# Kernel tuning notes

Hardware: AMD Instinct MI355X
Metric: run time of the kernel (lower is better)

The kernel has to match this reference:

```python
import jax, jax.numpy as jnp
import numpy as np

N_STREAMS = 8
DIM = 1024
N_HEADS = 16
HEAD_DIM = DIM // N_HEADS
STREAM_DIM = DIM // N_STREAMS
EPS = 1e-6


def setup_inputs() -> dict:
    key = jax.random.key(0)
    ks = jax.random.split(key, 20)
    B, S, D = 2, 2048, DIM
    inp = {
        "x": jax.random.normal(ks[0], (B, S, D), jnp.float32),
        "rope_cos": jax.random.uniform(ks[1], (S, HEAD_DIM), jnp.float32),
        "rope_sin": jax.random.uniform(ks[2], (S, HEAD_DIM), jnp.float32),
        # DeltaOperator: learned per-channel decay logits
        "delta_decay": jax.random.normal(ks[3], (D,), jnp.float32) * 0.02,
        # gate_proj: Linear(D, 3*n)
        "gate_w": jax.random.normal(ks[4], (3 * N_STREAMS, D), jnp.float32) * 0.02,
        "gate_b": jnp.zeros((3 * N_STREAMS,), jnp.float32),
        "phi_res": jax.random.normal(ks[5], (N_STREAMS, N_STREAMS), jnp.float32) * 0.02,
        "ln1_w": jnp.ones((D,), jnp.float32),
        "ln2_w": jnp.ones((D,), jnp.float32),
        # MLP (StrategicLinear == Linear at inference)
        "w1": jax.random.normal(ks[6], (4 * D, D), jnp.float32) * 0.02,
        "b1": jnp.zeros((4 * D,), jnp.float32),
        "w2": jax.random.normal(ks[7], (D, 4 * D), jnp.float32) * 0.02,
        "b2": jnp.zeros((D,), jnp.float32),
        # nn.MultiheadAttention params
        "in_proj_w": jax.random.normal(ks[8], (3 * D, D), jnp.float32) * 0.02,
        "in_proj_b": jnp.zeros((3 * D,), jnp.float32),
        "out_w": jax.random.normal(ks[9], (D, D), jnp.float32) * 0.02,
        "out_b": jnp.zeros((D,), jnp.float32),
    }
    return inp


def delta_operator(x, decay_logits):
    # out_t = x_t - s_{t-1};  s_t = beta*s_{t-1} + (1-beta)*x_t  (per-channel EMA delta)
    beta = jax.nn.sigmoid(decay_logits)  # [D]

    def step(s, xt):
        out = xt - s
        s_new = beta * s + (1.0 - beta) * xt
        return s_new, out

    xT = jnp.swapaxes(x, 0, 1)  # [S,B,D]
    s0 = jnp.zeros_like(xT[0])
    _, ysT = jax.lax.scan(step, s0, xT)
    return jnp.swapaxes(ysT, 0, 1)  # [B,S,D]


def rms_norm(x, w):
    var = jnp.mean(x * x, axis=-1, keepdims=True)
    return x * jax.lax.rsqrt(var + EPS) * w


def sinkhorn_knopp(phi, iterations=15):
    K = jnp.exp(phi)
    for _ in range(iterations):
        K = K / jnp.sum(K, axis=1, keepdims=True)
        K = K / jnp.sum(K, axis=0, keepdims=True)
    return K


def causal_mha(x, in_proj_w, in_proj_b, out_w, out_b):
    B, S, D = x.shape
    qkv = x @ in_proj_w.T + in_proj_b  # [B,S,3D]
    q, k, v = jnp.split(qkv, 3, axis=-1)
    def heads(t):
        return t.reshape(B, S, N_HEADS, HEAD_DIM).transpose(0, 2, 1, 3)  # [B,H,S,hd]
    q, k, v = heads(q), heads(k), heads(v)
    scores = jnp.einsum("bhqd,bhkd->bhqk", q, k) / jnp.sqrt(jnp.float32(HEAD_DIM))
    mask = jnp.tril(jnp.ones((S, S), bool))
    scores = jnp.where(mask, scores, jnp.float32(-1e9))
    attn = jax.nn.softmax(scores, axis=-1)
    o = jnp.einsum("bhqk,bhkd->bhqd", attn, v)
    o = o.transpose(0, 2, 1, 3).reshape(B, S, D)
    return o @ out_w.T + out_b


def reference(x, rope_cos, rope_sin, delta_decay, gate_w, gate_b, phi_res,
              ln1_w, ln2_w, w1, b1, w2, b2, in_proj_w, in_proj_b, out_w, out_b):
    B, S, D = x.shape
    n = N_STREAMS
    x_delta = delta_operator(x, delta_decay)
    x_state = jnp.mean(x_delta, axis=1)  # [B,D]
    gates = x_state @ gate_w.T + gate_b  # [B,3n]
    g_res = jax.nn.sigmoid(gates[:, 2 * n:])[:, None, :, None]  # [B,1,n,1]
    H_res = sinkhorn_knopp(phi_res, 15)
    x_streams = x_delta.reshape(B, S, n, STREAM_DIM)
    # (x_perm @ H.T).permute back == einsum over stream axis
    mhc_out = jnp.einsum("bsnd,mn->bsmd", x_streams * g_res, H_res).reshape(B, S, D)
    normed = rms_norm(x_delta, ln1_w)
    attn_out = causal_mha(normed, in_proj_w, in_proj_b, out_w, out_b)
    normed2 = rms_norm(x_delta + attn_out, ln2_w)
    h = jax.nn.gelu(normed2 @ w1.T + b1, approximate=False)
    ffn_out = h @ w2.T + b2
    return x_delta + attn_out + ffn_out + mhc_out
```

## Files before the change

kernel.cpp:

```cpp
#include <hip/hip_runtime.h>
#include <hip/hip_bf16.h>
#include <math.h>

#define BB 2
#define SS 2048
#define DDIM 1024
#define NHEAD 16
#define NSTR 8
#define SDIMC 128
#define NCH 16
#define CLEN 128
#define EPSV 1e-6f

using bf16 = __hip_bfloat16;
typedef __attribute__((ext_vector_type(8))) __bf16 bf8;
typedef __attribute__((ext_vector_type(4))) __bf16 bf4v;
typedef __attribute__((ext_vector_type(4))) float f4;

__device__ __forceinline__ bf16 f2b(float v) { return __float2bfloat16(v); }
__device__ __forceinline__ bf8 ld8(const bf16* p) { return *(const bf8*)p; }
__device__ __forceinline__ f4 MFMA(bf8 a, bf8 b, f4 c) {
  return __builtin_amdgcn_mfma_f32_16x16x32_bf16(a, b, c, 0, 0, 0);
}
__device__ __forceinline__ float sigm(float x) { return 1.0f / (1.0f + expf(-x)); }
__device__ __forceinline__ float fexp2(float x) { return __builtin_amdgcn_exp2f(x); }

__device__ __forceinline__ float gelu_f(float v) {
  float x = v * 0.70710678118654752f;
  float ax = fabsf(x);
  float t = __builtin_amdgcn_rcpf(1.0f + 0.3275911f * ax);
  float p = ((((1.061405429f * t - 1.453152027f) * t + 1.421413741f) * t
              - 0.284496736f) * t + 0.254829592f) * t;
  float e = 1.0f - p * fexp2(-ax * ax * 1.4426950408889634f);
  e = copysignf(e, x);
  return 0.5f * v * (1.0f + e);
}

__device__ __forceinline__ void glds16(bf16* l, const bf16* g) {
  __builtin_amdgcn_global_load_lds(
      (const __attribute__((address_space(1))) unsigned int*)g,
      (__attribute__((address_space(3))) unsigned int*)l, 16, 0, 0);
}

__global__ __launch_bounds__(256) void cvt_all(const float* __restrict__ ipw,
                                               const float* __restrict__ ow,
                                               const float* __restrict__ w1,
                                               const float* __restrict__ w2,
                                               bf16* __restrict__ WIPW,
                                               bf16* __restrict__ WOW,
                                               bf16* __restrict__ W1B,
                                               bf16* __restrict__ W2B) {
  const int S1 = 3 * DDIM * DDIM, S2 = S1 + DDIM * DDIM,
            S3 = S2 + 4 * DDIM * DDIM;
  int i4 = (blockIdx.x * 256 + threadIdx.x) * 4;
  const float* src;
  bf16* dst;
  int off;
  if (i4 < S1)      { src = ipw; dst = WIPW; off = i4; }
  else if (i4 < S2) { src = ow;  dst = WOW;  off = i4 - S1; }
  else if (i4 < S3) { src = w1;  dst = W1B;  off = i4 - S2; }
  else              { src = w2;  dst = W2B;  off = i4 - S3; }
  float4 v = *(const float4*)(src + off);
  bf4v o;
  o[0] = (__bf16)v.x; o[1] = (__bf16)v.y; o[2] = (__bf16)v.z; o[3] = (__bf16)v.w;
  *(bf4v*)(dst + off) = o;
}

__global__ __launch_bounds__(256) void delta_passA(const float* __restrict__ x,
                                                   const float* __restrict__ decay,
                                                   float* __restrict__ SA) {
  int idx = blockIdx.x * 256 + threadIdx.x;
  int d = idx % DDIM;
  int c = (idx / DDIM) % NCH;
  int b = idx / (DDIM * NCH);
  float beta = sigm(decay[d]);
  float omb = 1.0f - beta;
  const float* xp = x + ((size_t)(b * SS + c * CLEN)) * DDIM + d;
  float s = 0.0f;
  for (int j = 0; j < CLEN; j++) {
    float xv = xp[(size_t)j * DDIM];
    s = beta * s + omb * xv;
  }
  SA[idx] = s;
}

__global__ __launch_bounds__(256) void delta_passB(const float* __restrict__ SA,
                                                   const float* __restrict__ decay,
                                                   float* __restrict__ SIN) {
  int idx = blockIdx.x * 256 + threadIdx.x;
  int d = idx % DDIM;
  int b = idx / DDIM;
  float beta = sigm(decay[d]);
  float p = beta;
  for (int i = 0; i < 7; i++) p *= p;
  float s = 0.0f;
  for (int c = 0; c < NCH; c++) {
    SIN[(b * NCH + c) * DDIM + d] = s;
    s = p * s + SA[(b * NCH + c) * DDIM + d];
  }
}

__global__ __launch_bounds__(256) void delta_passC(const float* __restrict__ x,
                                                   const float* __restrict__ decay,
                                                   const float* __restrict__ SIN,
                                                   float* __restrict__ XD,
                                                   float* __restrict__ SA) {
  int idx = blockIdx.x * 256 + threadIdx.x;
  int d = idx % DDIM;
  int c = (idx / DDIM) % NCH;
  int b = idx / (DDIM * NCH);
  float beta = sigm(decay[d]);
  float omb = 1.0f - beta;
  const float* xp = x + ((size_t)(b * SS + c * CLEN)) * DDIM + d;
  float* xdp = XD + ((size_t)(b * SS + c * CLEN)) * DDIM + d;
  float s = SIN[idx];
  float sum = 0.0f;
  for (int j = 0; j < CLEN; j++) {
    float xv = xp[(size_t)j * DDIM];
    float o = xv - s;
    xdp[(size_t)j * DDIM] = o;
    sum += o;
    s = beta * s + omb * xv;
  }
  SA[idx] = sum;
}

__global__ __launch_bounds__(1024) void gates_sinkhorn(const float* __restrict__ SA,
                                                       const float* __restrict__ gw,
                                                       const float* __restrict__ gb,
                                                       const float* __restrict__ phi,
                                                       float* __restrict__ gres,
                                                       float* __restrict__ hres) {
  int tid = threadIdx.x;
  int wave = tid >> 6, lane = tid & 63;
  int b = wave >> 3, j = wave & 7;
  float acc = 0.0f;
  for (int d = lane; d < DDIM; d += 64) {
    float xs = 0.0f;
    for (int c = 0; c < NCH; c++) xs += SA[(b * NCH + c) * DDIM + d];
    xs *= (1.0f / (float)SS);
    acc += xs * gw[(2 * NSTR + j) * DDIM + d];
  }
  for (int off = 32; off > 0; off >>= 1) acc += __shfl_down(acc, off);
  if (lane == 0) gres[b * NSTR + j] = sigm(acc + gb[2 * NSTR + j]);
  __syncthreads();
  if (tid == 0) {
    float Km[8][8];
    for (int i = 0; i < 8; i++)
      for (int jj = 0; jj < 8; jj++) Km[i][jj] = expf(phi[i * 8 + jj]);
    for (int it = 0; it < 15; it++) {
      for (int i = 0; i < 8; i++) {
        float rs = 0.0f;
        for (int jj = 0; jj < 8; jj++) rs += Km[i][jj];
        float inv = 1.0f / rs;
        for (int jj = 0; jj < 8; jj++) Km[i][jj] *= inv;
      }
      for (int jj = 0; jj < 8; jj++) {
        float cs = 0.0f;
        for (int i = 0; i < 8; i++) cs += Km[i][jj];
        float inv = 1.0f / cs;
        for (int i = 0; i < 8; i++) Km[i][jj] *= inv;
      }
    }
    for (int i = 0; i < 8; i++)
      for (int jj = 0; jj < 8; jj++) hres[i * 8 + jj] = Km[i][jj];
  }
}

__global__ __launch_bounds__(256) void rmsnorm_k(const float* __restrict__ in,
                                                 const float* __restrict__ w,
                                                 bf16* __restrict__ out) {
  int row = blockIdx.x;
  const float* r = in + (size_t)row * DDIM;
  int tid = threadIdx.x;
  float ss = 0.0f;
  for (int i = tid; i < DDIM; i += 256) {
    float v = r[i];
    ss += v * v;
  }
  for (int off = 32; off > 0; off >>= 1) ss += __shfl_down(ss, off);
  __shared__ float red[4];
  if ((tid & 63) == 0) red[tid >> 6] = ss;
  __syncthreads();
  float tot = red[0] + red[1] + red[2] + red[3];
  float sc = rsqrtf(tot / (float)DDIM + EPSV);
  bf16* o = out + (size_t)row * DDIM;
  for (int i = tid; i < DDIM; i += 256) o[i] = f2b(r[i] * sc * w[i]);
}

template <int ODT, int EPI>
__global__ __launch_bounds__(256) void gemm_lds(const bf16* __restrict__ A,
                                                const bf16* __restrict__ W,
                                                const float* __restrict__ bias,
                                                const float* __restrict__ res,
                                                void* __restrict__ outp,
                                                int M, int N, int K) {
  __shared__ bf16 As[2][128 * 32];
  __shared__ bf16 Bs[2][128 * 32];
  int tid = threadIdx.x;
  int lane = tid & 63, wv = tid >> 6;
  int ml = lane & 15, quad = lane >> 4;
  int wr = wv >> 1, wc = wv & 1;
  int m0 = blockIdx.x * 128, n0 = blockIdx.y * 128;
  const bf16* ga[2];
  const bf16* gb[2];
  int lofs[2];
#pragma unroll
  for (int it = 0; it < 2; it++) {
    int c = it * 256 + tid;
    int row = c >> 2, kc = (c & 3) * 8;
    ga[it] = A + (size_t)(m0 + row) * K + kc;
    gb[it] = W + (size_t)(n0 + row) * K + kc;
    lofs[it] = c * 8;
  }
#pragma unroll
  for (int it = 0; it < 2; it++) {
    glds16(&As[0][lofs[it]], ga[it]);
    glds16(&Bs[0][lofs[it]], gb[it]);
  }
  f4 acc[4][4] = {};
  int nk = K >> 5;
  int cur = 0;
  __syncthreads();
  for (int t = 0; t < nk; t++) {
    if (t + 1 < nk) {
      int ko = (t + 1) * 32;
#pragma unroll
      for (int it = 0; it < 2; it++) {
        glds16(&As[cur ^ 1][lofs[it]], ga[it] + ko);
        glds16(&Bs[cur ^ 1][lofs[it]], gb[it] + ko);
      }
    }
    bf8 af[4], bfr[4];
#pragma unroll
    for (int mi = 0; mi < 4; mi++)
      af[mi] = ld8(&As[cur][(wr * 64 + mi * 16 + ml) * 32 + quad * 8]);
#pragma unroll
    for (int ni = 0; ni < 4; ni++)
      bfr[ni] = ld8(&Bs[cur][(wc * 64 + ni * 16 + ml) * 32 + quad * 8]);
#pragma unroll
    for (int mi = 0; mi < 4; mi++)
#pragma unroll
      for (int ni = 0; ni < 4; ni++)
        acc[mi][ni] = MFMA(af[mi], bfr[ni], acc[mi][ni]);
    __syncthreads();
    cur ^= 1;
  }
#pragma unroll
  for (int mi = 0; mi < 4; mi++)
#pragma unroll
    for (int ni = 0; ni < 4; ni++)
#pragma unroll
      for (int r = 0; r < 4; r++) {
        int row = m0 + wr * 64 + mi * 16 + quad * 4 + r;
        int col = n0 + wc * 64 + ni * 16 + ml;
        size_t idx = (size_t)row * N + col;
        float v = acc[mi][ni][r] + bias[col];
        if (EPI == 1) v = gelu_f(v);
        if (EPI == 2) v += res[idx];
        if (ODT == 1) ((bf16*)outp)[idx] = f2b(v);
        else ((float*)outp)[idx] = v;
      }
}

__global__ __launch_bounds__(256) void gemm_part2(const bf16* __restrict__ A,
                                                  const bf16* __restrict__ W,
                                                  float* __restrict__ P0,
                                                  float* __restrict__ P1,
                                                  int M, int N, int KS, int LDK) {
  __shared__ bf16 As[2][128 * 32];
  __shared__ bf16 Bs[2][128 * 32];
  int tid = threadIdx.x;
  int lane = tid & 63, wv = tid >> 6;
  int ml = lane & 15, quad = lane >> 4;
  int wr = wv >> 1, wc = wv & 1;
  int m0 = blockIdx.x * 128, n0 = blockIdx.y * 128;
  const bf16* Ab = A + blockIdx.z * KS;
  const bf16* Wb = W + blockIdx.z * KS;
  float* P = blockIdx.z ? P1 : P0;
  const bf16* ga[2];
  const bf16* gb[2];
  int lofs[2];
#pragma unroll
  for (int it = 0; it < 2; it++) {
    int c = it * 256 + tid;
    int row = c >> 2, kc = (c & 3) * 8;
    ga[it] = Ab + (size_t)(m0 + row) * LDK + kc;
    gb[it] = Wb + (size_t)(n0 + row) * LDK + kc;
    lofs[it] = c * 8;
  }
#pragma unroll
  for (int it = 0; it < 2; it++) {
    glds16(&As[0][lofs[it]], ga[it]);
    glds16(&Bs[0][lofs[it]], gb[it]);
  }
  f4 acc[4][4] = {};
  int nk = KS >> 5;
  int cur = 0;
  __syncthreads();
  for (int t = 0; t < nk; t++) {
    if (t + 1 < nk) {
      int ko = (t + 1) * 32;
#pragma unroll
      for (int it = 0; it < 2; it++) {
        glds16(&As[cur ^ 1][lofs[it]], ga[it] + ko);
        glds16(&Bs[cur ^ 1][lofs[it]], gb[it] + ko);
      }
    }
    bf8 af[4], bfr[4];
#pragma unroll
    for (int mi = 0; mi < 4; mi++)
      af[mi] = ld8(&As[cur][(wr * 64 + mi * 16 + ml) * 32 + quad * 8]);
#pragma unroll
    for (int ni = 0; ni < 4; ni++)
      bfr[ni] = ld8(&Bs[cur][(wc * 64 + ni * 16 + ml) * 32 + quad * 8]);
#pragma unroll
    for (int mi = 0; mi < 4; mi++)
#pragma unroll
      for (int ni = 0; ni < 4; ni++)
        acc[mi][ni] = MFMA(af[mi], bfr[ni], acc[mi][ni]);
    __syncthreads();
    cur ^= 1;
  }
#pragma unroll
  for (int mi = 0; mi < 4; mi++)
#pragma unroll
    for (int ni = 0; ni < 4; ni++)
#pragma unroll
      for (int r = 0; r < 4; r++) {
        int row = m0 + wr * 64 + mi * 16 + quad * 4 + r;
        int col = n0 + wc * 64 + ni * 16 + ml;
        P[(size_t)row * N + col] = acc[mi][ni][r];
      }
}

template <int ODT, int EPI>
__global__ __launch_bounds__(256) void gemm_lds64(const bf16* __restrict__ A,
                                                  const bf16* __restrict__ W,
                                                  const float* __restrict__ bias,
                                                  const float* __restrict__ res,
                                                  void* __restrict__ outp,
                                                  int M, int N, int K) {
  __shared__ bf16 As[2][64 * 32];
  __shared__ bf16 Bs[2][128 * 32];
  int tid = threadIdx.x;
  int lane = tid & 63, wv = tid >> 6;
  int ml = lane & 15, quad = lane >> 4;
  int wr = wv & 1, wc = wv >> 1;
  int m0 = blockIdx.x * 64, n0 = blockIdx.y * 128;
  const bf16* gaA;
  const bf16* gb[2];
  int lofA, lofs[2];
  {
    int c = tid;
    int row = c >> 2, kc = (c & 3) * 8;
    gaA = A + (size_t)(m0 + row) * K + kc;
    lofA = c * 8;
  }
#pragma unroll
  for (int it = 0; it < 2; it++) {
    int c = it * 256 + tid;
    int row = c >> 2, kc = (c & 3) * 8;
    gb[it] = W + (size_t)(n0 + row) * K + kc;
    lofs[it] = c * 8;
  }
  glds16(&As[0][lofA], gaA);
#pragma unroll
  for (int it = 0; it < 2; it++) glds16(&Bs[0][lofs[it]], gb[it]);
  f4 acc[2][4] = {};
  int nk = K >> 5;
  int cur = 0;
  __syncthreads();
  for (int t = 0; t < nk; t++) {
    if (t + 1 < nk) {
      int ko = (t + 1) * 32;
      glds16(&As[cur ^ 1][lofA], gaA + ko);
#pragma unroll
      for (int it = 0; it < 2; it++) glds16(&Bs[cur ^ 1][lofs[it]], gb[it] + ko);
    }
    bf8 af[2], bfr[4];
#pragma unroll
    for (int mi = 0; mi < 2; mi++)
      af[mi] = ld8(&As[cur][(wr * 32 + mi * 16 + ml) * 32 + quad * 8]);
#pragma unroll
    for (int ni = 0; ni < 4; ni++)
      bfr[ni] = ld8(&Bs[cur][(wc * 64 + ni * 16 + ml) * 32 + quad * 8]);
#pragma unroll
    for (int mi = 0; mi < 2; mi++)
#pragma unroll
      for (int ni = 0; ni < 4; ni++)
        acc[mi][ni] = MFMA(af[mi], bfr[ni], acc[mi][ni]);
    __syncthreads();
    cur ^= 1;
  }
#pragma unroll
  for (int mi = 0; mi < 2; mi++)
#pragma unroll
    for (int ni = 0; ni < 4; ni++)
#pragma unroll
      for (int r = 0; r < 4; r++) {
        int row = m0 + wr * 32 + mi * 16 + quad * 4 + r;
        int col = n0 + wc * 64 + ni * 16 + ml;
        size_t idx = (size_t)row * N + col;
        float v = acc[mi][ni][r] + bias[col];
        if (EPI == 1) v = gelu_f(v);
        if (EPI == 2) v += res[idx];
        if (ODT == 1) ((bf16*)outp)[idx] = f2b(v);
        else ((float*)outp)[idx] = v;
      }
}

__global__ __launch_bounds__(256) void vtrans(const bf16* __restrict__ qkv,
                                              bf16* __restrict__ VT) {
  int bid = blockIdx.x;
  int st = bid % (SS / 64);
  int h = (bid / (SS / 64)) % NHEAD;
  int b = bid / ((SS / 64) * NHEAD);
  __shared__ bf16 tile[64][65];
  int s0 = st * 64;
  int tid = threadIdx.x;
  for (int it = 0; it < 16; it++) {
    int sl = it * 4 + (tid >> 6), dl = tid & 63;
    tile[sl][dl] = qkv[(size_t)(b * SS + s0 + sl) * (3 * DDIM) + 2 * DDIM + h * 64 + dl];
  }
  __syncthreads();
  for (int it = 0; it < 16; it++) {
    int dl = it * 4 + (tid >> 6), sl = tid & 63;
    VT[((size_t)(b * NHEAD + h) * 64 + dl) * SS + s0 + sl] = tile[sl][dl];
  }
}

__device__ __forceinline__ void qk_softmax(bool active, int kt, int q0, int nkt,
                                           const bf8 kf[4][2], const bf8* qf,
                                           f4* oacc, float& m, float& l,
                                           bf8* pf, bf16 (*pl)[72],
                                           int ml, int quad, int k0) {
  if (!active) return;
  const float SC = 0.125f * 1.44269504089f;
  f4 s[4] = {{0,0,0,0},{0,0,0,0},{0,0,0,0},{0,0,0,0}};
  __builtin_amdgcn_s_setprio(1);
#pragma unroll
  for (int kk = 0; kk < 2; kk++)
#pragma unroll
    for (int c = 0; c < 4; c++)
      s[c] = MFMA(kf[c][kk], qf[kk], s[c]);
  __builtin_amdgcn_s_setprio(0);
  if (kt == nkt - 1) {
    int qi = q0 + ml;
#pragma unroll
    for (int c = 0; c < 4; c++)
#pragma unroll
      for (int r = 0; r < 4; r++)
        if (k0 + c * 16 + quad * 4 + r > qi) s[c][r] = -1e30f;
  }
  float mx = s[0][0];
#pragma unroll
  for (int c = 0; c < 4; c++)
#pragma unroll
    for (int r = 0; r < 4; r++) mx = fmaxf(mx, s[c][r]);
  mx = fmaxf(mx, __shfl_xor(mx, 16));
  mx = fmaxf(mx, __shfl_xor(mx, 32));
  float mn = fmaxf(m, mx * SC);
  float alpha = fexp2(m - mn);
  float rs = 0.0f;
  float p[4][4];
#pragma unroll
  for (int c = 0; c < 4; c++)
#pragma unroll
    for (int r = 0; r < 4; r++) {
      p[c][r] = fexp2(__builtin_fmaf(s[c][r], SC, -mn));
      rs += p[c][r];
    }
  rs += __shfl_xor(rs, 16);
  rs += __shfl_xor(rs, 32);
  l = l * alpha + rs;
  m = mn;
  float alr[4];
#pragma unroll
  for (int r = 0; r < 4; r++) alr[r] = __shfl(alpha, quad * 4 + r);
#pragma unroll
  for (int c = 0; c < 4; c++)
#pragma unroll
    for (int r = 0; r < 4; r++) oacc[c][r] *= alr[r];
#pragma unroll
  for (int c = 0; c < 4; c++) {
    bf4v w;
#pragma unroll
    for (int r = 0; r < 4; r++) w[r] = (__bf16)p[c][r];
    *(bf4v*)&pl[ml][c * 16 + quad * 4] = w;
  }
#pragma unroll
  for (int kk = 0; kk < 2; kk++) pf[kk] = ld8(&pl[ml][kk * 32 + quad * 8]);
}

__device__ __forceinline__ void pv_acc(bool active, const bf8* pf,
                                       const bf8 vf[4][2], f4* oacc) {
  if (!active) return;
  __builtin_amdgcn_s_setprio(1);
#pragma unroll
  for (int c = 0; c < 4; c++)
#pragma unroll
    for (int kk = 0; kk < 2; kk++)
      oacc[c] = MFMA(pf[kk], vf[c][kk], oacc[c]);
  __builtin_amdgcn_s_setprio(0);
}

__global__ __launch_bounds__(256) void flash_attn(const bf16* __restrict__ qkv,
                                                  const bf16* __restrict__ VT,
                                                  bf16* __restrict__ obuf) {
  int rb = blockIdx.x;
  int bid = (rb & 7) * 64 + (rb >> 3);
  int j = bid & 15;
  int blk = (j & 1) ? (15 - (j >> 1)) : (j >> 1);
  int h = (bid >> 4) & 15;
  int b = bid >> 8;
  int tid = threadIdx.x;
  int wv = tid >> 6, lane = tid & 63;
  int ml = lane & 15, quad = lane >> 4;
  int idx0 = blk * 4 + wv;
  int idx1 = 127 - idx0;
  int q0a = idx0 * 16, q0b = idx1 * 16;
  int nkt0 = blk + 1;
  int nkt1 = 32 - blk;
  int maxn = nkt1;

  __shared__ __align__(16) bf16 Ks[2][64 * 64];
  __shared__ __align__(16) bf16 Vs[2][64 * 64];
  __shared__ __align__(16) bf16 plds[4][2][16][72];
  bf16 (*plA)[72] = plds[wv][0];
  bf16 (*plB)[72] = plds[wv][1];

  bf8 qfa[2], qfb[2];
#pragma unroll
  for (int kk = 0; kk < 2; kk++) {
    qfa[kk] = ld8(qkv + (size_t)(b * SS + q0a + ml) * (3 * DDIM) + h * 64 + kk * 32 + quad * 8);
    qfb[kk] = ld8(qkv + (size_t)(b * SS + q0b + ml) * (3 * DDIM) + h * 64 + kk * 32 + quad * 8);
  }
  f4 oacca[4] = {{0,0,0,0},{0,0,0,0},{0,0,0,0},{0,0,0,0}};
  f4 oaccb[4] = {{0,0,0,0},{0,0,0,0},{0,0,0,0},{0,0,0,0}};
  float ma = -1e30f, la = 0.0f, mb = -1e30f, lb = 0.0f;

  const bf16* kglob = qkv + (size_t)b * SS * (3 * DDIM) + DDIM + h * 64;
  const bf16* vglob = VT + (size_t)(b * NHEAD + h) * 64 * SS;

#pragma unroll
  for (int it = 0; it < 2; it++) {
    int lam = it * 256 + tid;
    int row = lam >> 3;
    int ch = (lam & 7) ^ (row & 7);
    glds16(&Ks[0][lam * 8], kglob + (size_t)row * (3 * DDIM) + ch * 8);
    glds16(&Vs[0][lam * 8], vglob + (size_t)row * SS + ch * 8);
  }
  __syncthreads();
  int cur = 0;
  for (int kt = 0; kt < maxn; kt++) {
    int k0 = kt * 64;
    if (kt + 1 < maxn) {
      int k0n = (kt + 1) * 64;
#pragma unroll
      for (int it = 0; it < 2; it++) {
        int lam = it * 256 + tid;
        int row = lam >> 3;
        int ch = (lam & 7) ^ (row & 7);
        glds16(&Ks[cur ^ 1][lam * 8], kglob + (size_t)(k0n + row) * (3 * DDIM) + ch * 8);
        glds16(&Vs[cur ^ 1][lam * 8], vglob + (size_t)row * SS + k0n + ch * 8);
      }
    }
    bool act0 = kt < nkt0;
    bf8 kf[4][2];
#pragma unroll
    for (int kk = 0; kk < 2; kk++)
#pragma unroll
      for (int c = 0; c < 4; c++) {
        int chunk = ((c * 16 + ml) << 3) + ((kk * 4 + quad) ^ (ml & 7));
        kf[c][kk] = ld8(&Ks[cur][chunk * 8]);
      }
    bf8 pfa[2], pfb[2];
    qk_softmax(act0, kt, q0a, nkt0, kf, qfa, oacca, ma, la, pfa, plA, ml, quad, k0);
    qk_softmax(true, kt, q0b, nkt1, kf, qfb, oaccb, mb, lb, pfb, plB, ml, quad, k0);
    bf8 vf[4][2];
#pragma unroll
    for (int kk = 0; kk < 2; kk++)
#pragma unroll
      for (int c = 0; c < 4; c++) {
        int chunk = ((c * 16 + ml) << 3) + ((kk * 4 + quad) ^ (ml & 7));
        vf[c][kk] = ld8(&Vs[cur][chunk * 8]);
      }
    pv_acc(act0, pfa, vf, oacca);
    pv_acc(true, pfb, vf, oaccb);
    __syncthreads();
    cur ^= 1;
  }
  float lna[4], lnb[4];
#pragma unroll
  for (int r = 0; r < 4; r++) {
    lna[r] = __shfl(la, quad * 4 + r);
    lnb[r] = __shfl(lb, quad * 4 + r);
  }
#pragma unroll
  for (int c = 0; c < 4; c++)
#pragma unroll
    for (int r = 0; r < 4; r++) {
      int rowa = q0a + quad * 4 + r;
      int rowb = q0b + quad * 4 + r;
      obuf[(size_t)(b * SS + rowa) * DDIM + h * 64 + c * 16 + ml] =
          f2b(oacca[c][r] / lna[r]);
      obuf[(size_t)(b * SS + rowb) * DDIM + h * 64 + c * 16 + ml] =
          f2b(oaccb[c][r] / lnb[r]);
    }
}

__global__ __launch_bounds__(256) void final_k(const float* __restrict__ y,
                                               const float* __restrict__ P0,
                                               const float* __restrict__ P1,
                                               const float* __restrict__ bias,
                                               const float* __restrict__ xd,
                                               const float* __restrict__ hres,
                                               const float* __restrict__ gres,
                                               float* __restrict__ out) {
  int row = blockIdx.x;
  int b = row / SS;
  int tid = threadIdx.x;
  __shared__ float cf[8][8];
  if (tid < 64) cf[tid >> 3][tid & 7] = hres[tid] * gres[b * NSTR + (tid & 7)];
  __syncthreads();
  const float* yr = y + (size_t)row * DDIM;
  const float* p0 = P0 + (size_t)row * DDIM;
  const float* p1 = P1 + (size_t)row * DDIM;
  const float* xr = xd + (size_t)row * DDIM;
  float* o = out + (size_t)row * DDIM;
  for (int i = tid; i < DDIM; i += 256) {
    int m = i >> 7, dd = i & 127;
    float acc = yr[i] + p0[i] + p1[i] + bias[i];
#pragma unroll
    for (int n = 0; n < 8; n++) acc += cf[m][n] * xr[n * SDIMC + dd];
    o[i] = acc;
  }
}

extern "C" void kernel_launch(void* const* d_in, const int* in_sizes, int n_in,
                              void* d_out, int out_size, void* d_ws, size_t ws_size,
                              hipStream_t stream) {
  const float* x     = (const float*)d_in[0];
  const float* decay = (const float*)d_in[3];
  const float* gw    = (const float*)d_in[4];
  const float* gb    = (const float*)d_in[5];
  const float* phi   = (const float*)d_in[6];
  const float* ln1   = (const float*)d_in[7];
  const float* ln2   = (const float*)d_in[8];
  const float* w1    = (const float*)d_in[9];
  const float* b1    = (const float*)d_in[10];
  const float* w2    = (const float*)d_in[11];
  const float* b2    = (const float*)d_in[12];
  const float* ipw   = (const float*)d_in[13];
  const float* ipb   = (const float*)d_in[14];
  const float* ow    = (const float*)d_in[15];
  const float* obs   = (const float*)d_in[16];
  float* out = (float*)d_out;

  const size_t MB = 1048576ull;
  char* wsp = (char*)d_ws;
  float* SA   = (float*)(wsp);
  float* SIN  = (float*)(wsp + 131072ull);
  float* GRES = (float*)(wsp + 262144ull);
  float* HRES = (float*)(wsp + 262208ull);
  float* XD   = (float*)(wsp + 1 * MB);
  float* AO   = (float*)(wsp + 17 * MB);
  bf16*  NORM = (bf16*)(wsp + 33 * MB);
  bf16*  OB   = (bf16*)(wsp + 41 * MB);
  bf16*  QKV  = (bf16*)(wsp + 49 * MB);
  bf16*  VT   = (bf16*)(wsp + 73 * MB);
  bf16*  HB   = (bf16*)(wsp + 49 * MB);
  bf16*  WIPW = (bf16*)(wsp + 81 * MB);
  bf16*  WOW  = (bf16*)(wsp + 87 * MB);
  bf16*  W1B  = (bf16*)(wsp + 89 * MB);
  bf16*  W2B  = (bf16*)(wsp + 97 * MB);
  float* PK0  = (float*)(wsp + 33 * MB);
  float* PK1  = (float*)(wsp + 81 * MB);

  cvt_all<<<dim3(12 * DDIM * DDIM / 1024), dim3(256), 0, stream>>>(
      ipw, ow, w1, w2, WIPW, WOW, W1B, W2B);

  delta_passA<<<dim3(BB * NCH * DDIM / 256), dim3(256), 0, stream>>>(x, decay, SA);
  delta_passB<<<dim3(BB * DDIM / 256), dim3(256), 0, stream>>>(SA, decay, SIN);
  delta_passC<<<dim3(BB * NCH * DDIM / 256), dim3(256), 0, stream>>>(x, decay, SIN, XD, SA);
  gates_sinkhorn<<<dim3(1), dim3(1024), 0, stream>>>(SA, gw, gb, phi, GRES, HRES);
  rmsnorm_k<<<dim3(BB * SS), dim3(256), 0, stream>>>(XD, ln1, NORM);
  gemm_lds<1, 0><<<dim3(32, 24), dim3(256), 0, stream>>>(NORM, WIPW, ipb, nullptr,
                                                         QKV, BB * SS, 3 * DDIM, DDIM);
  vtrans<<<dim3(BB * NHEAD * (SS / 64)), dim3(256), 0, stream>>>(QKV, VT);
  flash_attn<<<dim3(BB * NHEAD * 16), dim3(256), 0, stream>>>(QKV, VT, OB);
  gemm_lds64<0, 2><<<dim3(64, 8), dim3(256), 0, stream>>>(OB, WOW, obs, XD,
                                                          AO, BB * SS, DDIM, DDIM);
  rmsnorm_k<<<dim3(BB * SS), dim3(256), 0, stream>>>(AO, ln2, NORM);
  gemm_lds<1, 1><<<dim3(32, 32), dim3(256), 0, stream>>>(NORM, W1B, b1, nullptr,
                                                         HB, BB * SS, 4 * DDIM, DDIM);
  gemm_part2<<<dim3(32, 8, 2), dim3(256), 0, stream>>>(HB, W2B, PK0, PK1,
                                                       BB * SS, DDIM, 2 * DDIM, 4 * DDIM);
  final_k<<<dim3(BB * SS), dim3(256), 0, stream>>>(AO, PK0, PK1, b2, XD,
                                                   HRES, GRES, out);
}
```

Before: 425.6 us.

## Triple-buffer GEMM LDS tiles with two-stage prefetch and partial vmcnt waits

Converts the three GEMM kernels from double-buffered to triple-buffered LDS staging. Tiles are prefetched two K-steps ahead, and the full __syncthreads is replaced with an s_waitcnt vmcnt(N) plus s_barrier, so the newest prefetch stays in flight across the barrier. This is meant to hide more global-load latency behind MFMA work. The cost is 50% more LDS per block, which may reduce occupancy, and the hand-counted vmcnt values must match the number of outstanding loads for the code to stay correct.

Measured after the change: 432.7 us. Within noise of the previous version (+1.7%).

```diff
diff --git a/kernel.cpp b/kernel.cpp
--- a/kernel.cpp
+++ b/kernel.cpp
@@ -195,8 +195,8 @@
                                                 const float* __restrict__ res,
                                                 void* __restrict__ outp,
                                                 int M, int N, int K) {
-  __shared__ bf16 As[2][128 * 32];
-  __shared__ bf16 Bs[2][128 * 32];
+  __shared__ bf16 As[3][128 * 32];
+  __shared__ bf16 Bs[3][128 * 32];
   int tid = threadIdx.x;
   int lane = tid & 63, wv = tid >> 6;
   int ml = lane & 15, quad = lane >> 4;
@@ -218,17 +218,24 @@
     glds16(&As[0][lofs[it]], ga[it]);
     glds16(&Bs[0][lofs[it]], gb[it]);
   }
+#pragma unroll
+  for (int it = 0; it < 2; it++) {
+    glds16(&As[1][lofs[it]], ga[it] + 32);
+    glds16(&Bs[1][lofs[it]], gb[it] + 32);
+  }
   f4 acc[4][4] = {};
   int nk = K >> 5;
+  asm volatile("s_waitcnt vmcnt(4)" ::: "memory");
+  __builtin_amdgcn_s_barrier();
   int cur = 0;
-  __syncthreads();
   for (int t = 0; t < nk; t++) {
-    if (t + 1 < nk) {
-      int ko = (t + 1) * 32;
+    if (t + 2 < nk) {
+      int ko = (t + 2) * 32;
+      int nb = cur + 2; if (nb >= 3) nb -= 3;
 #pragma unroll
       for (int it = 0; it < 2; it++) {
-        glds16(&As[cur ^ 1][lofs[it]], ga[it] + ko);
-        glds16(&Bs[cur ^ 1][lofs[it]], gb[it] + ko);
+        glds16(&As[nb][lofs[it]], ga[it] + ko);
+        glds16(&Bs[nb][lofs[it]], gb[it] + ko);
       }
     }
     bf8 af[4], bfr[4];
@@ -243,8 +250,14 @@
 #pragma unroll
       for (int ni = 0; ni < 4; ni++)
         acc[mi][ni] = MFMA(af[mi], bfr[ni], acc[mi][ni]);
-    __syncthreads();
-    cur ^= 1;
+    if (t + 2 < nk) {
+      asm volatile("s_waitcnt vmcnt(4)" ::: "memory");
+      __builtin_amdgcn_s_barrier();
+    } else if (t + 1 < nk) {
+      asm volatile("s_waitcnt vmcnt(0)" ::: "memory");
+      __builtin_amdgcn_s_barrier();
+    }
+    cur++; if (cur >= 3) cur = 0;
   }
 #pragma unroll
   for (int mi = 0; mi < 4; mi++)
@@ -268,8 +281,8 @@
                                                   float* __restrict__ P0,
                                                   float* __restrict__ P1,
                                                   int M, int N, int KS, int LDK) {
-  __shared__ bf16 As[2][128 * 32];
-  __shared__ bf16 Bs[2][128 * 32];
+  __shared__ bf16 As[3][128 * 32];
+  __shared__ bf16 Bs[3][128 * 32];
   int tid = threadIdx.x;
   int lane = tid & 63, wv = tid >> 6;
   int ml = lane & 15, quad = lane >> 4;
@@ -294,17 +307,24 @@
     glds16(&As[0][lofs[it]], ga[it]);
     glds16(&Bs[0][lofs[it]], gb[it]);
   }
+#pragma unroll
+  for (int it = 0; it < 2; it++) {
+    glds16(&As[1][lofs[it]], ga[it] + 32);
+    glds16(&Bs[1][lofs[it]], gb[it] + 32);
+  }
   f4 acc[4][4] = {};
   int nk = KS >> 5;
+  asm volatile("s_waitcnt vmcnt(4)" ::: "memory");
+  __builtin_amdgcn_s_barrier();
   int cur = 0;
-  __syncthreads();
   for (int t = 0; t < nk; t++) {
-    if (t + 1 < nk) {
-      int ko = (t + 1) * 32;
+    if (t + 2 < nk) {
+      int ko = (t + 2) * 32;
+      int nb = cur + 2; if (nb >= 3) nb -= 3;
 #pragma unroll
       for (int it = 0; it < 2; it++) {
-        glds16(&As[cur ^ 1][lofs[it]], ga[it] + ko);
-        glds16(&Bs[cur ^ 1][lofs[it]], gb[it] + ko);
+        glds16(&As[nb][lofs[it]], ga[it] + ko);
+        glds16(&Bs[nb][lofs[it]], gb[it] + ko);
       }
     }
     bf8 af[4], bfr[4];
@@ -319,8 +339,14 @@
 #pragma unroll
       for (int ni = 0; ni < 4; ni++)
         acc[mi][ni] = MFMA(af[mi], bfr[ni], acc[mi][ni]);
-    __syncthreads();
-    cur ^= 1;
+    if (t + 2 < nk) {
+      asm volatile("s_waitcnt vmcnt(4)" ::: "memory");
+      __builtin_amdgcn_s_barrier();
+    } else if (t + 1 < nk) {
+      asm volatile("s_waitcnt vmcnt(0)" ::: "memory");
+      __builtin_amdgcn_s_barrier();
+    }
+    cur++; if (cur >= 3) cur = 0;
   }
 #pragma unroll
   for (int mi = 0; mi < 4; mi++)
@@ -341,8 +367,8 @@
                                                   const float* __restrict__ res,
                                                   void* __restrict__ outp,
                                                   int M, int N, int K) {
-  __shared__ bf16 As[2][64 * 32];
-  __shared__ bf16 Bs[2][128 * 32];
+  __shared__ bf16 As[3][64 * 32];
+  __shared__ bf16 Bs[3][128 * 32];
   int tid = threadIdx.x;
   int lane = tid & 63, wv = tid >> 6;
   int ml = lane & 15, quad = lane >> 4;
@@ -367,16 +393,21 @@
   glds16(&As[0][lofA], gaA);
 #pragma unroll
   for (int it = 0; it < 2; it++) glds16(&Bs[0][lofs[it]], gb[it]);
+  glds16(&As[1][lofA], gaA + 32);
+#pragma unroll
+  for (int it = 0; it < 2; it++) glds16(&Bs[1][lofs[it]], gb[it] + 32);
   f4 acc[2][4] = {};
   int nk = K >> 5;
+  asm volatile("s_waitcnt vmcnt(3)" ::: "memory");
+  __builtin_amdgcn_s_barrier();
   int cur = 0;
-  __syncthreads();
   for (int t = 0; t < nk; t++) {
-    if (t + 1 < nk) {
-      int ko = (t + 1) * 32;
-      glds16(&As[cur ^ 1][lofA], gaA + ko);
-#pragma unroll
-      for (int it = 0; it < 2; it++) glds16(&Bs[cur ^ 1][lofs[it]], gb[it] + ko);
+    if (t + 2 < nk) {
+      int ko = (t + 2) * 32;
+      int nb = cur + 2; if (nb >= 3) nb -= 3;
+      glds16(&As[nb][lofA], gaA + ko);
+#pragma unroll
+      for (int it = 0; it < 2; it++) glds16(&Bs[nb][lofs[it]], gb[it] + ko);
     }
     bf8 af[2], bfr[4];
 #pragma unroll
@@ -390,8 +421,14 @@
 #pragma unroll
       for (int ni = 0; ni < 4; ni++)
         acc[mi][ni] = MFMA(af[mi], bfr[ni], acc[mi][ni]);
-    __syncthreads();
-    cur ^= 1;
+    if (t + 2 < nk) {
+      asm volatile("s_waitcnt vmcnt(3)" ::: "memory");
+      __builtin_amdgcn_s_barrier();
+    } else if (t + 1 < nk) {
+      asm volatile("s_waitcnt vmcnt(0)" ::: "memory");
+      __builtin_amdgcn_s_barrier();
+    }
+    cur++; if (cur >= 3) cur = 0;
   }
 #pragma unroll
   for (int mi = 0; mi < 2; mi++)
```

## Replace 128x128 GEMM with 256x256 swizzled-LDS pipelined kernel for QKV and FFN1

Applied to the files above, without the earlier changes.

Swaps the 128x128 tile bf16 GEMM used for the QKV projection and the first FFN layer for a 256x256-tile, 512-thread kernel. The new kernel uses BK=64, an XOR-swizzled LDS layout, staggered prefetch of A and B across sub-steps, explicit waitcnt and barrier control, s_setprio around the MFMA bursts, and an XCD-aware block remap. The aim is higher arithmetic intensity per LDS load and better overlap of global loads with MFMA work. The cost is larger LDS use and far fewer blocks (192 and 256), which risks underfilling the CUs and depends on fragile hand-written synchronisation.

After: 417.4 us. About the same (-1.9%).

```diff
diff --git a/kernel.cpp b/kernel.cpp
--- a/kernel.cpp
+++ b/kernel.cpp
@@ -188,79 +188,116 @@
   for (int i = tid; i < DDIM; i += 256) o[i] = f2b(r[i] * sc * w[i]);
 }
 
-template <int ODT, int EPI>
-__global__ __launch_bounds__(256) void gemm_lds(const bf16* __restrict__ A,
-                                                const bf16* __restrict__ W,
-                                                const float* __restrict__ bias,
-                                                const float* __restrict__ res,
-                                                void* __restrict__ outp,
-                                                int M, int N, int K) {
-  __shared__ bf16 As[2][128 * 32];
-  __shared__ bf16 Bs[2][128 * 32];
+template <int EPI>
+__global__ __launch_bounds__(512, 2) void gemm256(const bf16* __restrict__ Ag,
+                                                  const bf16* __restrict__ Wg,
+                                                  const float* __restrict__ bias,
+                                                  bf16* __restrict__ outp,
+                                                  int M, int N, int K, int nby) {
+  __shared__ __align__(16) bf16 As[2][16384];
+  __shared__ __align__(16) bf16 Bs[2][16384];
+  int nwg = gridDim.x;
+  int cpx = nwg >> 3;
+  int l = (blockIdx.x & 7) * cpx + (blockIdx.x >> 3);
+  int bm = l / nby, bn = l % nby;
+  int m0 = bm * 256, n0 = bn * 256;
   int tid = threadIdx.x;
   int lane = tid & 63, wv = tid >> 6;
   int ml = lane & 15, quad = lane >> 4;
-  int wr = wv >> 1, wc = wv & 1;
-  int m0 = blockIdx.x * 128, n0 = blockIdx.y * 128;
-  const bf16* ga[2];
-  const bf16* gb[2];
-  int lofs[2];
-#pragma unroll
-  for (int it = 0; it < 2; it++) {
-    int c = it * 256 + tid;
-    int row = c >> 2, kc = (c & 3) * 8;
-    ga[it] = A + (size_t)(m0 + row) * K + kc;
-    gb[it] = W + (size_t)(n0 + row) * K + kc;
-    lofs[it] = c * 8;
-  }
-#pragma unroll
-  for (int it = 0; it < 2; it++) {
-    glds16(&As[0][lofs[it]], ga[it]);
-    glds16(&Bs[0][lofs[it]], gb[it]);
-  }
-  f4 acc[4][4] = {};
-  int nk = K >> 5;
-  int cur = 0;
-  __syncthreads();
-  for (int t = 0; t < nk; t++) {
-    if (t + 1 < nk) {
-      int ko = (t + 1) * 32;
-#pragma unroll
-      for (int it = 0; it < 2; it++) {
-        glds16(&As[cur ^ 1][lofs[it]], ga[it] + ko);
-        glds16(&Bs[cur ^ 1][lofs[it]], gb[it] + ko);
-      }
+  int wrow = wv >> 2, wcol = wv & 3;
+
+  size_t aoff[2][2], boff[2][2];
+  int lof[2][2];
+#pragma unroll
+  for (int h = 0; h < 2; h++)
+#pragma unroll
+    for (int j = 0; j < 2; j++) {
+      int b = tid * 16 + j * 8192;
+      int s = b >> 10, w = b & 1023;
+      int wl = w ^ (((w >> 9) & 1) << 5);
+      int row = h * 128 + (s >> 1) * 16 + (wl >> 6);
+      int col = (s & 1) * 32 + ((wl & 63) >> 1);
+      aoff[h][j] = (size_t)(m0 + row) * K + col;
+      boff[h][j] = (size_t)(n0 + row) * K + col;
+      lof[h][j] = (h * 16384 + b) >> 1;
     }
-    bf8 af[4], bfr[4];
-#pragma unroll
-    for (int mi = 0; mi < 4; mi++)
-      af[mi] = ld8(&As[cur][(wr * 64 + mi * 16 + ml) * 32 + quad * 8]);
+  int wq2 = ((((ml << 6) + (quad << 4)) ^ (((int)(ml >= 8)) << 5))) >> 1;
+
+#define SA_(c, kt, h) { glds16(&As[c][lof[h][0]], Ag + aoff[h][0] + (size_t)(kt) * 64); \
+                        glds16(&As[c][lof[h][1]], Ag + aoff[h][1] + (size_t)(kt) * 64); }
+#define SB_(c, kt, h) { glds16(&Bs[c][lof[h][0]], Wg + boff[h][0] + (size_t)(kt) * 64); \
+                        glds16(&Bs[c][lof[h][1]], Wg + boff[h][1] + (size_t)(kt) * 64); }
+
+  SA_(0, 0, 0); SA_(0, 0, 1);
+  SB_(0, 0, 0); SB_(0, 0, 1);
+  SB_(1, 1, 0); SB_(1, 1, 1);
+  f4 acc[8][4] = {};
+  asm volatile("s_waitcnt vmcnt(4)" ::: "memory");
+  __builtin_amdgcn_s_barrier();
+  asm volatile("" ::: "memory");
+
+  int T = K >> 6;
+  for (int t = 0; t < T; t++) {
+    int c = t & 1;
+    bf8 bfrag[4][2];
+#pragma unroll
+    for (int q = 0; q < 4; q++) {
+      bf8 af[2][2];
+#pragma unroll
+      for (int mi2 = 0; mi2 < 2; mi2++)
+#pragma unroll
+        for (int kk = 0; kk < 2; kk++)
+          af[mi2][kk] =
+              ld8(&As[c][(((wrow * 8 + q * 2 + mi2) * 2 + kk) << 9) + wq2]);
+      if (q == 0) {
+#pragma unroll
+        for (int ni = 0; ni < 4; ni++)
+#pragma unroll
+          for (int kk = 0; kk < 2; kk++)
+            bfrag[ni][kk] =
+                ld8(&Bs[c][(((wcol * 4 + ni) * 2 + kk) << 9) + wq2]);
+      }
+      if (q == 0 && t + 1 < T) SA_(c ^ 1, t + 1, 0);
+      if (q == 1 && t + 1 < T) SA_(c ^ 1, t + 1, 1);
+      if (q == 2 && t + 2 < T) SB_(c, t + 2, 0);
+      if (q == 3 && t + 2 < T) SB_(c, t + 2, 1);
+      __builtin_amdgcn_s_barrier();
+      asm volatile("s_waitcnt lgkmcnt(0)" ::: "memory");
+      __builtin_amdgcn_s_setprio(1);
+#pragma unroll
+      for (int mi2 = 0; mi2 < 2; mi2++)
+#pragma unroll
+        for (int ni = 0; ni < 4; ni++)
+#pragma unroll
+          for (int kk = 0; kk < 2; kk++)
+            acc[q * 2 + mi2][ni] =
+                MFMA(af[mi2][kk], bfrag[ni][kk], acc[q * 2 + mi2][ni]);
+      __builtin_amdgcn_s_setprio(0);
+      if (q == 3) {
+        if (t + 2 < T) {
+          asm volatile("s_waitcnt vmcnt(4)" ::: "memory");
+        } else if (t + 1 < T) {
+          asm volatile("s_waitcnt vmcnt(0)" ::: "memory");
+        }
+      }
+      __builtin_amdgcn_s_barrier();
+      asm volatile("" ::: "memory");
+    }
+  }
+#pragma unroll
+  for (int mi = 0; mi < 8; mi++)
 #pragma unroll
     for (int ni = 0; ni < 4; ni++)
-      bfr[ni] = ld8(&Bs[cur][(wc * 64 + ni * 16 + ml) * 32 + quad * 8]);
-#pragma unroll
-    for (int mi = 0; mi < 4; mi++)
-#pragma unroll
-      for (int ni = 0; ni < 4; ni++)
-        acc[mi][ni] = MFMA(af[mi], bfr[ni], acc[mi][ni]);
-    __syncthreads();
-    cur ^= 1;
-  }
-#pragma unroll
-  for (int mi = 0; mi < 4; mi++)
-#pragma unroll
-    for (int ni = 0; ni < 4; ni++)
 #pragma unroll
       for (int r = 0; r < 4; r++) {
-        int row = m0 + wr * 64 + mi * 16 + quad * 4 + r;
-        int col = n0 + wc * 64 + ni * 16 + ml;
-        size_t idx = (size_t)row * N + col;
+        int row = m0 + wrow * 128 + mi * 16 + quad * 4 + r;
+        int col = n0 + wcol * 64 + ni * 16 + ml;
         float v = acc[mi][ni][r] + bias[col];
         if (EPI == 1) v = gelu_f(v);
-        if (EPI == 2) v += res[idx];
-        if (ODT == 1) ((bf16*)outp)[idx] = f2b(v);
-        else ((float*)outp)[idx] = v;
-      }
+        outp[(size_t)row * N + col] = f2b(v);
+      }
+#undef SA_
+#undef SB_
 }
 
 __global__ __launch_bounds__(256) void gemm_part2(const bf16* __restrict__ A,
@@ -686,15 +723,15 @@
   delta_passC<<<dim3(BB * NCH * DDIM / 256), dim3(256), 0, stream>>>(x, decay, SIN, XD, SA);
   gates_sinkhorn<<<dim3(1), dim3(1024), 0, stream>>>(SA, gw, gb, phi, GRES, HRES);
   rmsnorm_k<<<dim3(BB * SS), dim3(256), 0, stream>>>(XD, ln1, NORM);
-  gemm_lds<1, 0><<<dim3(32, 24), dim3(256), 0, stream>>>(NORM, WIPW, ipb, nullptr,
-                                                         QKV, BB * SS, 3 * DDIM, DDIM);
+  gemm256<0><<<dim3(192), dim3(512), 0, stream>>>(NORM, WIPW, ipb, QKV,
+                                                  BB * SS, 3 * DDIM, DDIM, 12);
   vtrans<<<dim3(BB * NHEAD * (SS / 64)), dim3(256), 0, stream>>>(QKV, VT);
   flash_attn<<<dim3(BB * NHEAD * 16), dim3(256), 0, stream>>>(QKV, VT, OB);
   gemm_lds64<0, 2><<<dim3(64, 8), dim3(256), 0, stream>>>(OB, WOW, obs, XD,
                                                           AO, BB * SS, DDIM, DDIM);
   rmsnorm_k<<<dim3(BB * SS), dim3(256), 0, stream>>>(AO, ln2, NORM);
-  gemm_lds<1, 1><<<dim3(32, 32), dim3(256), 0, stream>>>(NORM, W1B, b1, nullptr,
-                                                         HB, BB * SS, 4 * DDIM, DDIM);
+  gemm256<1><<<dim3(256), dim3(512), 0, stream>>>(NORM, W1B, b1, HB,
+                                                  BB * SS, 4 * DDIM, DDIM, 16);
   gemm_part2<<<dim3(32, 8, 2), dim3(256), 0, stream>>>(HB, W2B, PK0, PK1,
                                                        BB * SS, DDIM, 2 * DDIM, 4 * DDIM);
   final_k<<<dim3(BB * SS), dim3(256), 0, stream>>>(AO, PK0, PK1, b2, XD,
```
